# Optimization experiments

Measured on AMD Instinct MI355X. Metric: run time of the kernel, lower is better.

Reference implementation:

```python
import jax, jax.numpy as jnp
import numpy as np

WS = 7          # window size (square)
SHIFT = 3       # shift size
NH = 8          # num heads
DIM = 256
B, H, W = 32, 56, 56


def _relative_position_index(ws: int) -> np.ndarray:
    coords = np.stack(np.meshgrid(np.arange(ws), np.arange(ws), indexing='ij'))  # (2, ws, ws)
    cf = coords.reshape(2, -1)                                                   # (2, N)
    rel = cf[:, :, None] - cf[:, None, :]                                        # (2, N, N)
    rel = rel.transpose(1, 2, 0).copy()
    rel[:, :, 0] += ws - 1
    rel[:, :, 1] += ws - 1
    rel[:, :, 0] *= 2 * ws - 1
    return rel.sum(-1).reshape(-1).astype(np.int32)                              # (N*N,)


def _shift_mask(h: int, w: int, ws: int, shift: int) -> np.ndarray:
    img = np.zeros((h, w), dtype=np.float32)
    cnt = 0
    for hs in ((0, -ws), (-ws, -shift), (-shift, None)):
        for wsl in ((0, -ws), (-ws, -shift), (-shift, None)):
            img[hs[0]:hs[1], wsl[0]:wsl[1]] = cnt
            cnt += 1
    nwh, nww = h // ws, w // ws
    m = img.reshape(nwh, ws, nww, ws).transpose(0, 2, 1, 3).reshape(nwh * nww, ws * ws)
    am = m[:, None, :] - m[:, :, None]                 # (nW, N, N)
    return np.where(am != 0, np.float32(-100.0), np.float32(0.0))


def setup_inputs() -> dict:
    key = jax.random.key(0)
    ks = jax.random.split(key, 5)
    x = jax.random.normal(ks[0], (B, H, W, DIM), jnp.float32)
    qkv_weight = jax.random.normal(ks[1], (3 * DIM, DIM), jnp.float32) * 0.02
    qkv_bias = jnp.zeros((3 * DIM,), jnp.float32)
    proj_weight = jax.random.normal(ks[2], (DIM, DIM), jnp.float32) * 0.02
    proj_bias = jnp.zeros((DIM,), jnp.float32)
    rel_bias_table = jax.random.normal(ks[3], ((2 * WS - 1) ** 2, NH), jnp.float32) * 0.02
    rel_pos_index = jnp.asarray(_relative_position_index(WS))
    return {
        'x': x, 'qkv_weight': qkv_weight, 'qkv_bias': qkv_bias,
        'proj_weight': proj_weight, 'proj_bias': proj_bias,
        'rel_bias_table': rel_bias_table, 'rel_pos_index': rel_pos_index,
    }


def reference(x, qkv_weight, qkv_bias, proj_weight, proj_bias, rel_bias_table, rel_pos_index):
    b, h, w, c = x.shape
    n = WS * WS
    hd = c // NH
    nwh, nww = h // WS, w // WS
    nw = nwh * nww

    # relative position bias: (1, NH, N, N)
    bias = rel_bias_table[rel_pos_index].reshape(n, n, NH).transpose(2, 0, 1)[None]

    # cyclic shift
    xs = jnp.roll(x, (-SHIFT, -SHIFT), axis=(1, 2))

    # window partition -> (B*nW, N, C)
    xw = xs.reshape(b, nwh, WS, nww, WS, c).transpose(0, 1, 3, 2, 4, 5).reshape(b * nw, n, c)

    qkv = xw @ qkv_weight.T + qkv_bias
    qkv = qkv.reshape(b * nw, n, 3, NH, hd).transpose(2, 0, 3, 1, 4)  # (3, B*nW, NH, N, hd)
    q = qkv[0] * (hd ** -0.5)
    k = qkv[1]
    v = qkv[2]

    attn = jnp.einsum('bhnd,bhmd->bhnm', q, k) + bias                # (B*nW, NH, N, N)

    # shift mask (static)
    amask = jnp.asarray(_shift_mask(h, w, WS, SHIFT))                # (nW, N, N)
    attn = attn.reshape(b, nw, NH, n, n) + amask[None, :, None]
    attn = jax.nn.softmax(attn.reshape(b * nw, NH, n, n), axis=-1)

    out = jnp.einsum('bhnm,bhmd->bhnd', attn, v)                     # (B*nW, NH, N, hd)
    out = out.transpose(0, 2, 1, 3).reshape(b * nw, n, c)
    out = out @ proj_weight.T + proj_bias

    # window reverse + reverse shift
    out = out.reshape(b, nwh, nww, WS, WS, c).transpose(0, 1, 3, 2, 4, 5).reshape(b, h, w, c)
    out = jnp.roll(out, (SHIFT, SHIFT), axis=(1, 2))
    return out
```

## Files before the change

### kernel.cpp

```cpp
#include <hip/hip_runtime.h>
#include <hip/hip_bf16.h>


#define NTOK 49
#define DIM_ 256
#define NH_  8
#define NQKV 196608
#define NPRJ 65536
#define NTABP 131072

#define WSP_B  393216ull
#define TAB_B  524288ull
#define Q_B    1048576ull
#define NEED_BIG 162312448ull
#define NEED_TAB (TAB_B + (unsigned long long)NTABP * 4)

typedef short v8s __attribute__((ext_vector_type(8)));
typedef float v4f __attribute__((ext_vector_type(4)));
typedef float v16f __attribute__((ext_vector_type(16)));

#define MFMA16 __builtin_amdgcn_mfma_f32_16x16x32_bf16
#define MFMA32 __builtin_amdgcn_mfma_f32_32x32x16_bf16
#define LGKM_WAIT() asm volatile("s_waitcnt lgkmcnt(0)" ::: "memory")

static __device__ __forceinline__ v8s zero_v8s() {
    v8s z = {0, 0, 0, 0, 0, 0, 0, 0};
    return z;
}

static __device__ __forceinline__ v16f zero_v16f() {
    v16f z;
    #pragma unroll
    for (int i = 0; i < 16; ++i) z[i] = 0.0f;
    return z;
}

static __device__ __forceinline__ v8s lds_frag(const __hip_bfloat16* p, int row,
                                               int stride, int koff, int nrows) {
    if (row < nrows) return *(const v8s*)(p + row * stride + koff);
    return zero_v8s();
}

static __device__ __forceinline__ v8s cvt8(const float* p) {
    v4f a = *(const v4f*)p;
    v4f b = *(const v4f*)(p + 4);
    union { v8s v; __hip_bfloat16 h[8]; } r;
    r.h[0] = __float2bfloat16(a[0]); r.h[1] = __float2bfloat16(a[1]);
    r.h[2] = __float2bfloat16(a[2]); r.h[3] = __float2bfloat16(a[3]);
    r.h[4] = __float2bfloat16(b[0]); r.h[5] = __float2bfloat16(b[1]);
    r.h[6] = __float2bfloat16(b[2]); r.h[7] = __float2bfloat16(b[3]);
    return r.v;
}

__global__ __launch_bounds__(256) void prep_kernel(
    const float* __restrict__ qkvW, const float* __restrict__ projW,
    const float* __restrict__ rbt, const int* __restrict__ rpi,
    __hip_bfloat16* __restrict__ wsQ, __hip_bfloat16* __restrict__ wsP,
    float* __restrict__ tabP, int doTab)
{
    int i = blockIdx.x * 256 + threadIdx.x;
    if (i < NQKV) { wsQ[i] = __float2bfloat16(qkvW[i]); return; }
    int j = i - NQKV;
    if (j < NPRJ) { wsP[j] = __float2bfloat16(projW[j]); return; }
    int t = j - NPRJ;
    if (!doTab || t >= NTABP) return;
    int cls = t >> 15;
    int rem = t & 32767;
    int h = rem >> 12;
    int p = rem & 4095;
    int row = p >> 6, col = p & 63;
    float val = -1e30f;
    if (row < NTOK && col < NTOK) {
        int rh = (cls & 1) ? (((row / 7) < 4) ? 1 : 2) : 0;
        int rw = (cls & 2) ? (((row % 7) < 4) ? 1 : 2) : 0;
        int ch = (cls & 1) ? (((col / 7) < 4) ? 1 : 2) : 0;
        int cw = (cls & 2) ? (((col % 7) < 4) ? 1 : 2) : 0;
        float mask = ((rh * 3 + rw) != (ch * 3 + cw)) ? -100.0f : 0.0f;
        val = rbt[rpi[row * 49 + col] * NH_ + h] + mask;
    }
    tabP[t] = val;
}

__global__ __launch_bounds__(256) void qkvattn_kernel(
    const float* __restrict__ x,
    const float* __restrict__ qkvB,
    const __hip_bfloat16* __restrict__ wsQ,
    const float* __restrict__ tabP,
    __hip_bfloat16* __restrict__ OH)
{
    constexpr int SXS = 264;
    constexpr int QKS = 40;
    constexpr int VTS = 72;
    constexpr int PS  = 72;
    constexpr int WVSZ = 2 * NTOK * QKS + 32 * VTS;

    __shared__ alignas(16) __hip_bfloat16 s_x[NTOK * SXS];
    __shared__ alignas(16) __hip_bfloat16 s_wv[4 * WVSZ];

    const int tid = threadIdx.x, wave = tid >> 6, lane = tid & 63;
    const int quad = lane >> 4, l16 = lane & 15;
    const int l32 = lane & 31, half = lane >> 5;
    const int win = blockIdx.x;
    const int b = win >> 6, wh = (win >> 3) & 7, wwi = win & 7;
    const int cls = ((wh == 7) ? 1 : 0) | ((wwi == 7) ? 2 : 0);

    __hip_bfloat16* wq  = s_wv + wave * WVSZ;
    __hip_bfloat16* wk  = wq + NTOK * QKS;
    __hip_bfloat16* wvt = wq + 2 * NTOK * QKS;
    __hip_bfloat16* wp  = wq;

    for (int i = lane; i < 32 * 7; i += 64)
        wvt[(i / 7) * VTS + 49 + (i % 7)] = __float2bfloat16(0.0f);

    for (int i = tid; i < NTOK * 64; i += 256) {
        int tok = i >> 6, f4 = (i & 63) * 4;
        int r = tok / 7, c = tok - r * 7;
        int hg = wh * 7 + r + 3; if (hg >= 56) hg -= 56;
        int wg = wwi * 7 + c + 3; if (wg >= 56) wg -= 56;
        float4 v = *(const float4*)(x + ((b * 56 + hg) * 56 + wg) * DIM_ + f4);
        __hip_bfloat16* dst = s_x + tok * SXS + f4;
        dst[0] = __float2bfloat16(v.x);
        dst[1] = __float2bfloat16(v.y);
        dst[2] = __float2bfloat16(v.z);
        dst[3] = __float2bfloat16(v.w);
    }
    __syncthreads();

    const float qscale = 0.17677669529663687f;
    const int r1 = (32 + l32 < NTOK) ? (32 + l32) : 0;
    const __hip_bfloat16* arow0 = s_x + l32 * SXS + half * 8;
    const __hip_bfloat16* arow1 = s_x + r1 * SXS + half * 8;

    for (int hp = 0; hp < 2; ++hp) {
        const int h = wave * 2 + hp;

        #pragma unroll
        for (int m = 0; m < 3; ++m) {
            const int nb = m * 256 + h * 32;
            const __hip_bfloat16* wrow = wsQ + (nb + l32) * DIM_ + half * 8;
            v16f acc0 = zero_v16f(), acc1 = zero_v16f();

            if (m < 2) {
                #pragma unroll
                for (int kh = 0; kh < 2; ++kh) {
                    v8s wf[8];
                    #pragma unroll
                    for (int k = 0; k < 8; ++k)
                        wf[k] = *(const v8s*)(wrow + kh * 128 + k * 16);
                    #pragma unroll
                    for (int k = 0; k < 8; ++k) {
                        v8s a0 = *(const v8s*)(arow0 + kh * 128 + k * 16);
                        v8s a1 = *(const v8s*)(arow1 + kh * 128 + k * 16);
                        acc0 = MFMA32(a0, wf[k], acc0, 0, 0, 0);
                        acc1 = MFMA32(a1, wf[k], acc1, 0, 0, 0);
                    }
                }
                float bias = qkvB[nb + l32];
                float sc = (m == 0) ? qscale : 1.0f;
                __hip_bfloat16* dst = (m == 0) ? wq : wk;
                #pragma unroll
                for (int rg = 0; rg < 16; ++rg) {
                    int rowoff = (rg & 3) + 8 * (rg >> 2) + 4 * half;
                    dst[rowoff * QKS + l32] =
                        __float2bfloat16((acc0[rg] + bias) * sc);
                    int tok1 = 32 + rowoff;
                    if (tok1 < NTOK)
                        dst[tok1 * QKS + l32] =
                            __float2bfloat16((acc1[rg] + bias) * sc);
                }
            } else {
                #pragma unroll
                for (int kh = 0; kh < 2; ++kh) {
                    v8s wf[8];
                    #pragma unroll
                    for (int k = 0; k < 8; ++k)
                        wf[k] = *(const v8s*)(wrow + kh * 128 + k * 16);
                    #pragma unroll
                    for (int k = 0; k < 8; ++k) {
                        v8s b0 = *(const v8s*)(arow0 + kh * 128 + k * 16);
                        v8s b1 = *(const v8s*)(arow1 + kh * 128 + k * 16);
                        acc0 = MFMA32(wf[k], b0, acc0, 0, 0, 0);
                        acc1 = MFMA32(wf[k], b1, acc1, 0, 0, 0);
                    }
                }
                const int tok1 = 32 + l32;
                #pragma unroll
                for (int rg = 0; rg < 16; ++rg) {
                    int feat = (rg & 3) + 8 * (rg >> 2) + 4 * half;
                    float bias = qkvB[nb + feat];
                    wvt[feat * VTS + l32] = __float2bfloat16(acc0[rg] + bias);
                    if (tok1 < NTOK)
                        wvt[feat * VTS + tok1] = __float2bfloat16(acc1[rg] + bias);
                }
            }
        }
        LGKM_WAIT();

        const float* tabh = tabP + (cls * NH_ + h) * 4096;
        __hip_bfloat16* qs = OH + (win * NH_ + h) * (NTOK * 32);

        v8s qa[4], kb[4];
        #pragma unroll
        for (int mt = 0; mt < 4; ++mt) {
            qa[mt] = lds_frag(wq, mt * 16 + l16, QKS, quad * 8, NTOK);
            kb[mt] = lds_frag(wk, mt * 16 + l16, QKS, quad * 8, NTOK);
        }
        v8s pb[2][2];
        #pragma unroll
        for (int nt = 0; nt < 2; ++nt) {
            const __hip_bfloat16* vr = wvt + (nt * 16 + l16) * VTS;
            pb[nt][0] = *(const v8s*)(vr + quad * 8);
            pb[nt][1] = (quad == 3) ? zero_v8s() : *(const v8s*)(vr + 32 + quad * 8);
        }
        LGKM_WAIT();

        #pragma unroll
        for (int ntq = 0; ntq < 4; ++ntq) {
            const int qtok = ntq * 16 + l16;
            v4f tv[4];
            #pragma unroll
            for (int mt = 0; mt < 4; ++mt)
                tv[mt] = *(const v4f*)(tabh + qtok * 64 + mt * 16 + quad * 4);
            v4f st[4];
            #pragma unroll
            for (int mt = 0; mt < 4; ++mt) {
                v4f z = {0.f, 0.f, 0.f, 0.f};
                st[mt] = MFMA16(kb[mt], qa[ntq], z, 0, 0, 0);
            }
            float v[16];
            float rmax = -1e30f;
            #pragma unroll
            for (int mt = 0; mt < 4; ++mt)
                #pragma unroll
                for (int rg = 0; rg < 4; ++rg) {
                    float s = st[mt][rg] + tv[mt][rg];
                    v[mt * 4 + rg] = s;
                    rmax = fmaxf(rmax, s);
                }
            rmax = fmaxf(rmax, __shfl_xor(rmax, 16, 64));
            rmax = fmaxf(rmax, __shfl_xor(rmax, 32, 64));
            float rsum = 0.f;
            #pragma unroll
            for (int i = 0; i < 16; ++i) {
                float e = (v[i] <= -1e29f) ? 0.f : __expf(v[i] - rmax);
                v[i] = e;
                rsum += e;
            }
            rsum += __shfl_xor(rsum, 16, 64);
            rsum += __shfl_xor(rsum, 32, 64);
            if (qtok < NTOK) {
                float inv = 1.0f / rsum;
                #pragma unroll
                for (int mt = 0; mt < 4; ++mt) {
                    union { __hip_bfloat16 h4[4]; unsigned long long u; } pk;
                    #pragma unroll
                    for (int rg = 0; rg < 4; ++rg)
                        pk.h4[rg] = __float2bfloat16(v[mt * 4 + rg] * inv);
                    *(unsigned long long*)(wp + qtok * PS + mt * 16 + quad * 4) = pk.u;
                }
            }
        }
        LGKM_WAIT();

        #pragma unroll
        for (int mtile = 0; mtile < 4; ++mtile) {
            v8s pa0 = lds_frag(wp, mtile * 16 + l16, PS, quad * 8, NTOK);
            v8s pa1 = lds_frag(wp, mtile * 16 + l16, PS, 32 + quad * 8, NTOK);
            #pragma unroll
            for (int nt = 0; nt < 2; ++nt) {
                v4f z = {0.f, 0.f, 0.f, 0.f};
                v4f acc = MFMA16(pa0, pb[nt][0], z, 0, 0, 0);
                acc = MFMA16(pa1, pb[nt][1], acc, 0, 0, 0);
                #pragma unroll
                for (int rg = 0; rg < 4; ++rg) {
                    int tok = mtile * 16 + quad * 4 + rg;
                    if (tok < NTOK)
                        qs[tok * 32 + nt * 16 + l16] = __float2bfloat16(acc[rg]);
                }
            }
        }
        LGKM_WAIT();
    }
}

__global__ __launch_bounds__(256) void proj_kernel(
    const __hip_bfloat16* __restrict__ OH,
    const __hip_bfloat16* __restrict__ wsP,
    const float* __restrict__ projB,
    float* __restrict__ out)
{
    const int tid = threadIdx.x, wave = tid >> 6, lane = tid & 63;
    const int quad = lane >> 4, l16 = lane & 15;
    const int bid = blockIdx.x;
    const int wg = bid >> 2, tq = bid & 3;
    const int m0 = wave * 16;
    const int tokA = m0 + l16;

    int ooff[4][4];
    #pragma unroll
    for (int wl = 0; wl < 4; ++wl) {
        int win = wg * 4 + wl;
        int b = win >> 6, wh = (win >> 3) & 7, wwi = win & 7;
        #pragma unroll
        for (int rg = 0; rg < 4; ++rg) {
            int row = m0 + quad * 4 + rg;
            if (row < NTOK) {
                int r = row / 7, c = row - r * 7;
                int hg = wh * 7 + r + 3; if (hg >= 56) hg -= 56;
                int wgl = wwi * 7 + c + 3; if (wgl >= 56) wgl -= 56;
                ooff[wl][rg] = ((b * 56 + hg) * 56 + wgl) * DIM_;
            } else ooff[wl][rg] = -1;
        }
    }

    #pragma unroll
    for (int tt = 0; tt < 4; ++tt) {
        const int t = tq * 4 + tt;
        const __hip_bfloat16* wrow = wsP + (t * 16 + l16) * DIM_;
        v8s wf[8];
        #pragma unroll
        for (int ks = 0; ks < 8; ++ks)
            wf[ks] = *(const v8s*)(wrow + ks * 32 + quad * 8);
        float pbv = projB[t * 16 + l16];

        #pragma unroll
        for (int wl = 0; wl < 4; ++wl) {
            const __hip_bfloat16* ohw =
                OH + (size_t)(wg * 4 + wl) * (NH_ * NTOK * 32);
            v4f acc = {0.f, 0.f, 0.f, 0.f};
            #pragma unroll
            for (int ks = 0; ks < 8; ++ks) {
                v8s af = (tokA < NTOK)
                    ? *(const v8s*)(ohw + ks * (NTOK * 32) + tokA * 32 + quad * 8)
                    : zero_v8s();
                acc = MFMA16(af, wf[ks], acc, 0, 0, 0);
            }
            #pragma unroll
            for (int rg = 0; rg < 4; ++rg)
                if (ooff[wl][rg] >= 0)
                    out[ooff[wl][rg] + t * 16 + l16] = acc[rg] + pbv;
        }
    }
}

__global__ __launch_bounds__(256, 2) void swin_attn_fused(
    const float* __restrict__ x,
    const float* __restrict__ qkvB,
    const float* __restrict__ projB,
    const float* __restrict__ rbt,
    const int*   __restrict__ rpi,
    const __hip_bfloat16* __restrict__ wsQ,
    const __hip_bfloat16* __restrict__ wsP,
    const float* __restrict__ biasTab,
    float*       __restrict__ out)
{
    constexpr int QKS = 40;
    constexpr int VTS = 72;
    constexpr int PS  = 72;
    constexpr int OS  = 264;
    constexpr int WVSZ = 6224;

    __shared__ alignas(16) __hip_bfloat16 s_wv[4 * WVSZ];
    __shared__ alignas(16) __hip_bfloat16 s_o[NTOK * OS];
    __shared__ int s_off[NTOK];
    __shared__ int s_reg[NTOK];

    const int tid  = threadIdx.x;
    const int wave = tid >> 6;
    const int lane = tid & 63;
    const int quad = lane >> 4;
    const int l16  = lane & 15;

    const int wid  = blockIdx.x;
    const int b    = wid >> 6;
    const int wIdx = wid & 63;
    const int wh   = wIdx >> 3;
    const int wwi  = wIdx & 7;

    if (tid < NTOK) {
        int r = tid / 7, c = tid - r * 7;
        int hs = wh * 7 + r, ws = wwi * 7 + c;
        int hg = hs + 3; if (hg >= 56) hg -= 56;
        int wg = ws + 3; if (wg >= 56) wg -= 56;
        s_off[tid] = ((b * 56 + hg) * 56 + wg) * DIM_;
        int rh = (hs < 49) ? 0 : ((hs < 53) ? 1 : 2);
        int rw = (ws < 49) ? 0 : ((ws < 53) ? 1 : 2);
        s_reg[tid] = rh * 3 + rw;
    }

    __hip_bfloat16* wq  = s_wv + wave * WVSZ;
    __hip_bfloat16* wk  = wq + NTOK * QKS;
    __hip_bfloat16* wvt = wq + 2 * NTOK * QKS;
    __hip_bfloat16* wp  = wq;

    for (int i = lane; i < 32 * 15; i += 64) {
        int f = i / 15, kk = 49 + (i % 15);
        wvt[f * VTS + kk] = __float2bfloat16(0.0f);
    }
    __syncthreads();

    const float qscale = 0.17677669529663687f;

    for (int hp = 0; hp < 2; ++hp) {
        const int h = wave * 2 + hp;
        LGKM_WAIT();

        for (int mh = 0; mh < 2; ++mh) {
            const int mbase = mh * 32;
            v8s at[2][8];
            #pragma unroll
            for (int sub = 0; sub < 2; ++sub) {
                int tok = mbase + sub * 16 + l16;
                const float* xr = (tok < NTOK) ? (x + s_off[tok]) : nullptr;
                #pragma unroll
                for (int ks = 0; ks < 8; ++ks)
                    at[sub][ks] = xr ? cvt8(xr + ks * 32 + quad * 8) : zero_v8s();
            }
            #pragma unroll
            for (int t = 0; t < 6; ++t) {
                int mat = t >> 1, ntile = t & 1;
                int nout = mat * 256 + h * 32 + ntile * 16 + l16;
                const __hip_bfloat16* wrow = wsQ + nout * DIM_;
                v4f a0 = {0.f, 0.f, 0.f, 0.f}, a1 = {0.f, 0.f, 0.f, 0.f};
                #pragma unroll
                for (int ks = 0; ks < 8; ++ks) {
                    v8s bfr = *(const v8s*)(wrow + ks * 32 + quad * 8);
                    a0 = MFMA16(at[0][ks], bfr, a0, 0, 0, 0);
                    a1 = MFMA16(at[1][ks], bfr, a1, 0, 0, 0);
                }
                float bias  = qkvB[nout];
                float scale = (mat == 0) ? qscale : 1.0f;
                #pragma unroll
                for (int sub = 0; sub < 2; ++sub) {
                    v4f acc = sub ? a1 : a0;
                    #pragma unroll
                    for (int rg = 0; rg < 4; ++rg) {
                        int row = mbase + sub * 16 + quad * 4 + rg;
                        if (row < NTOK) {
                            float val = (acc[rg] + bias) * scale;
                            int col = ntile * 16 + l16;
                            __hip_bfloat16 bv = __float2bfloat16(val);
                            if (mat == 0)      wq[row * QKS + col] = bv;
                            else if (mat == 1) wk[row * QKS + col] = bv;
                            else               wvt[col * VTS + row] = bv;
                        }
                    }
                }
            }
        }
        LGKM_WAIT();

        v8s qa[4], kb[4];
        #pragma unroll
        for (int i = 0; i < 4; ++i) {
            qa[i] = lds_frag(wq, i * 16 + l16, QKS, quad * 8, NTOK);
            kb[i] = lds_frag(wk, i * 16 + l16, QKS, quad * 8, NTOK);
        }
        int regc[4];
        #pragma unroll
        for (int nt = 0; nt < 4; ++nt) {
            int col = nt * 16 + l16;
            regc[nt] = (col < NTOK) ? s_reg[col] : -1;
        }
        LGKM_WAIT();
        const float* tabh = biasTab ? (biasTab + h * 4096) : nullptr;
        #pragma unroll
        for (int mtile = 0; mtile < 4; ++mtile) {
            v4f sa[4];
            #pragma unroll
            for (int nt = 0; nt < 4; ++nt) {
                v4f z = {0.f, 0.f, 0.f, 0.f};
                sa[nt] = MFMA16(qa[mtile], kb[nt], z, 0, 0, 0);
            }
            #pragma unroll
            for (int rg = 0; rg < 4; ++rg) {
                int row = mtile * 16 + quad * 4 + rg;
                bool rok = row < NTOK;
                int rr = rok ? s_reg[row] : -2;
                float v[4];
                float rmax = -1e30f;
                #pragma unroll
                for (int nt = 0; nt < 4; ++nt) {
                    int col = nt * 16 + l16;
                    float s = -1e30f;
                    if (rok && col < NTOK) {
                        float bv = tabh ? tabh[row * 64 + col]
                                        : rbt[rpi[row * 49 + col] * NH_ + h];
                        s = sa[nt][rg] + bv;
                        if (rr != regc[nt]) s -= 100.0f;
                    }
                    v[nt] = s;
                    rmax = fmaxf(rmax, s);
                }
                #pragma unroll
                for (int mm = 8; mm >= 1; mm >>= 1)
                    rmax = fmaxf(rmax, __shfl_xor(rmax, mm, 64));
                float rsum = 0.f;
                #pragma unroll
                for (int nt = 0; nt < 4; ++nt) {
                    float e = (v[nt] <= -1e29f) ? 0.f : __expf(v[nt] - rmax);
                    v[nt] = e;
                    rsum += e;
                }
                #pragma unroll
                for (int mm = 8; mm >= 1; mm >>= 1)
                    rsum += __shfl_xor(rsum, mm, 64);
                if (rok) {
                    float inv = 1.0f / rsum;
                    #pragma unroll
                    for (int nt = 0; nt < 4; ++nt)
                        wp[row * PS + nt * 16 + l16] = __float2bfloat16(v[nt] * inv);
                }
            }
        }
        LGKM_WAIT();

        v8s pb[2][2];
        #pragma unroll
        for (int nt = 0; nt < 2; ++nt)
            #pragma unroll
            for (int ks = 0; ks < 2; ++ks)
                pb[nt][ks] = *(const v8s*)(wvt + (nt * 16 + l16) * VTS + ks * 32 + quad * 8);
        #pragma unroll
        for (int mtile = 0; mtile < 4; ++mtile) {
            v8s pa0 = lds_frag(wp, mtile * 16 + l16, PS, quad * 8, NTOK);
            v8s pa1 = lds_frag(wp, mtile * 16 + l16, PS, 32 + quad * 8, NTOK);
            #pragma unroll
            for (int nt = 0; nt < 2; ++nt) {
                v4f z = {0.f, 0.f, 0.f, 0.f};
                v4f acc = MFMA16(pa0, pb[nt][0], z, 0, 0, 0);
                acc = MFMA16(pa1, pb[nt][1], acc, 0, 0, 0);
                #pragma unroll
                for (int rg = 0; rg < 4; ++rg) {
                    int row = mtile * 16 + quad * 4 + rg;
                    if (row < NTOK)
                        s_o[row * OS + h * 32 + nt * 16 + l16] = __float2bfloat16(acc[rg]);
                }
            }
        }
    }
    __syncthreads();

    {
        int m0 = wave * 16;
        v8s af[8];
        #pragma unroll
        for (int ks = 0; ks < 8; ++ks)
            af[ks] = lds_frag(s_o, m0 + l16, OS, ks * 32 + quad * 8, NTOK);
        #pragma unroll
        for (int t = 0; t < 16; ++t) {
            const __hip_bfloat16* wrow = wsP + (t * 16 + l16) * DIM_;
            v4f acc = {0.f, 0.f, 0.f, 0.f};
            #pragma unroll
            for (int ks = 0; ks < 8; ++ks) {
                v8s bfr = *(const v8s*)(wrow + ks * 32 + quad * 8);
                acc = MFMA16(af[ks], bfr, acc, 0, 0, 0);
            }
            float pbv = projB[t * 16 + l16];
            #pragma unroll
            for (int rg = 0; rg < 4; ++rg) {
                int row = m0 + quad * 4 + rg;
                if (row < NTOK)
                    out[s_off[row] + t * 16 + l16] = acc[rg] + pbv;
            }
        }
    }
}

extern "C" void kernel_launch(void* const* d_in, const int* in_sizes, int n_in,
                              void* d_out, int out_size, void* d_ws, size_t ws_size,
                              hipStream_t stream) {
    const float* x     = (const float*)d_in[0];
    const float* qkvW  = (const float*)d_in[1];
    const float* qkvB  = (const float*)d_in[2];
    const float* projW = (const float*)d_in[3];
    const float* projB = (const float*)d_in[4];
    const float* rbt   = (const float*)d_in[5];
    const int*   rpi   = (const int*)d_in[6];
    float* o = (float*)d_out;

    __hip_bfloat16* wsQ = (__hip_bfloat16*)d_ws;
    __hip_bfloat16* wsP = (__hip_bfloat16*)((char*)d_ws + WSP_B);
    float* tabP         = (float*)((char*)d_ws + TAB_B);
    __hip_bfloat16* OH  = (__hip_bfloat16*)((char*)d_ws + Q_B);

    const int prepBlocks = (NQKV + NPRJ + NTABP + 255) / 256;

    if (ws_size >= NEED_BIG) {
        prep_kernel<<<prepBlocks, 256, 0, stream>>>(qkvW, projW, rbt, rpi,
                                                    wsQ, wsP, tabP, 1);
        qkvattn_kernel<<<2048, 256, 0, stream>>>(x, qkvB, wsQ, tabP, OH);
        proj_kernel<<<2048, 256, 0, stream>>>(OH, wsP, projB, o);
    } else {
        int doTab = (ws_size >= NEED_TAB) ? 1 : 0;
        prep_kernel<<<prepBlocks, 256, 0, stream>>>(qkvW, projW, rbt, rpi,
                                                    wsQ, wsP, tabP, doTab);
        swin_attn_fused<<<2048, 256, 0, stream>>>(x, qkvB, projB, rbt, rpi,
                                                  wsQ, wsP, doTab ? tabP : nullptr, o);
    }
}
```

Before: 475.5 us.

## Restructure proj kernel to one window per block and pack LDS stores

The projection kernel now gives each block a single window and a quarter of the output columns, launching four times as many blocks. Activation fragments are held in registers while weight fragments are streamed per output tile. A block-index remapping makes neighbouring blocks share weight rows. Separately, the input staging in the QKV kernel writes four bf16 values with one packed 8-byte LDS store instead of four scalar stores. The trade is more weight traffic per window in exchange for more parallelism and lower register pressure.

```diff
diff --git a/kernel.cpp b/kernel.cpp
--- a/kernel.cpp
+++ b/kernel.cpp
@@ -118,11 +118,12 @@
         int hg = wh * 7 + r + 3; if (hg >= 56) hg -= 56;
         int wg = wwi * 7 + c + 3; if (wg >= 56) wg -= 56;
         float4 v = *(const float4*)(x + ((b * 56 + hg) * 56 + wg) * DIM_ + f4);
-        __hip_bfloat16* dst = s_x + tok * SXS + f4;
-        dst[0] = __float2bfloat16(v.x);
-        dst[1] = __float2bfloat16(v.y);
-        dst[2] = __float2bfloat16(v.z);
-        dst[3] = __float2bfloat16(v.w);
+        union { ushort4 u4; __hip_bfloat16 h[4]; } pkst;
+        pkst.h[0] = __float2bfloat16(v.x);
+        pkst.h[1] = __float2bfloat16(v.y);
+        pkst.h[2] = __float2bfloat16(v.z);
+        pkst.h[3] = __float2bfloat16(v.w);
+        *(ushort4*)(s_x + tok * SXS + f4) = pkst.u4;
     }
     __syncthreads();
 
@@ -292,54 +293,47 @@
     const int tid = threadIdx.x, wave = tid >> 6, lane = tid & 63;
     const int quad = lane >> 4, l16 = lane & 15;
     const int bid = blockIdx.x;
-    const int wg = bid >> 2, tq = bid & 3;
+    const int win = (bid & 7) | ((bid >> 5) << 3);
+    const int tq  = (bid >> 3) & 3;
+    const int b = win >> 6, wh = (win >> 3) & 7, wwi = win & 7;
     const int m0 = wave * 16;
     const int tokA = m0 + l16;
 
-    int ooff[4][4];
+    const __hip_bfloat16* ohw = OH + (size_t)win * (NH_ * NTOK * 32);
+    v8s af[8];
     #pragma unroll
-    for (int wl = 0; wl < 4; ++wl) {
-        int win = wg * 4 + wl;
-        int b = win >> 6, wh = (win >> 3) & 7, wwi = win & 7;
-        #pragma unroll
-        for (int rg = 0; rg < 4; ++rg) {
-            int row = m0 + quad * 4 + rg;
-            if (row < NTOK) {
-                int r = row / 7, c = row - r * 7;
-                int hg = wh * 7 + r + 3; if (hg >= 56) hg -= 56;
-                int wgl = wwi * 7 + c + 3; if (wgl >= 56) wgl -= 56;
-                ooff[wl][rg] = ((b * 56 + hg) * 56 + wgl) * DIM_;
-            } else ooff[wl][rg] = -1;
-        }
+    for (int ks = 0; ks < 8; ++ks)
+        af[ks] = (tokA < NTOK)
+                   ? *(const v8s*)(ohw + ks * (NTOK * 32) + tokA * 32 + quad * 8)
+                   : zero_v8s();
+
+    int ooff[4];
+    #pragma unroll
+    for (int rg = 0; rg < 4; ++rg) {
+        int row = m0 + quad * 4 + rg;
+        if (row < NTOK) {
+            int r = row / 7, c = row - r * 7;
+            int hg = wh * 7 + r + 3; if (hg >= 56) hg -= 56;
+            int wg = wwi * 7 + c + 3; if (wg >= 56) wg -= 56;
+            ooff[rg] = ((b * 56 + hg) * 56 + wg) * DIM_;
+        } else ooff[rg] = -1;
     }
 
     #pragma unroll
     for (int tt = 0; tt < 4; ++tt) {
         const int t = tq * 4 + tt;
         const __hip_bfloat16* wrow = wsP + (t * 16 + l16) * DIM_;
-        v8s wf[8];
-        #pragma unroll
-        for (int ks = 0; ks < 8; ++ks)
-            wf[ks] = *(const v8s*)(wrow + ks * 32 + quad * 8);
+        v4f acc = {0.f, 0.f, 0.f, 0.f};
+        #pragma unroll
+        for (int ks = 0; ks < 8; ++ks) {
+            v8s wf = *(const v8s*)(wrow + ks * 32 + quad * 8);
+            acc = MFMA16(af[ks], wf, acc, 0, 0, 0);
+        }
         float pbv = projB[t * 16 + l16];
-
-        #pragma unroll
-        for (int wl = 0; wl < 4; ++wl) {
-            const __hip_bfloat16* ohw =
-                OH + (size_t)(wg * 4 + wl) * (NH_ * NTOK * 32);
-            v4f acc = {0.f, 0.f, 0.f, 0.f};
-            #pragma unroll
-            for (int ks = 0; ks < 8; ++ks) {
-                v8s af = (tokA < NTOK)
-                    ? *(const v8s*)(ohw + ks * (NTOK * 32) + tokA * 32 + quad * 8)
-                    : zero_v8s();
-                acc = MFMA16(af, wf[ks], acc, 0, 0, 0);
-            }
-            #pragma unroll
-            for (int rg = 0; rg < 4; ++rg)
-                if (ooff[wl][rg] >= 0)
-                    out[ooff[wl][rg] + t * 16 + l16] = acc[rg] + pbv;
-        }
+        #pragma unroll
+        for (int rg = 0; rg < 4; ++rg)
+            if (ooff[rg] >= 0)
+                out[ooff[rg] + t * 16 + l16] = acc[rg] + pbv;
     }
 }
 
@@ -590,7 +584,7 @@
         prep_kernel<<<prepBlocks, 256, 0, stream>>>(qkvW, projW, rbt, rpi,
                                                     wsQ, wsP, tabP, 1);
         qkvattn_kernel<<<2048, 256, 0, stream>>>(x, qkvB, wsQ, tabP, OH);
-        proj_kernel<<<2048, 256, 0, stream>>>(OH, wsP, projB, o);
+        proj_kernel<<<8192, 256, 0, stream>>>(OH, wsP, projB, o);
     } else {
         int doTab = (ws_size >= NEED_TAB) ? 1 : 0;
         prep_kernel<<<prepBlocks, 256, 0, stream>>>(qkvW, projW, rbt, rpi,
```

Result: no change. 467.0 us (-1.8%).
